# Performance work log

Measured on AMD Instinct MI355X. Metric: run time of the kernel, lower is better.

Reference implementation:

```python
import jax, jax.numpy as jnp
import numpy as np

NUM_HEADS = 32
NUM_KV_HEADS = 8  # num_heads // 4 (GQA)
HEAD_DIM = 64     # hidden_size // num_heads
ROPE_BASE = 10000.0


def _rotate_half(x):
    x1, x2 = jnp.split(x, 2, axis=-1)
    return jnp.concatenate((-x2, x1), axis=-1)


def _rope_cos_sin(seq_len, dtype):
    inv_freq = 1.0 / (ROPE_BASE ** (jnp.arange(0, HEAD_DIM, 2, dtype=jnp.float32) / HEAD_DIM))
    t = jnp.arange(seq_len, dtype=jnp.float32)
    freqs = jnp.outer(t, inv_freq)                 # [S, HEAD_DIM//2]
    emb = jnp.concatenate((freqs, freqs), axis=-1) # [S, HEAD_DIM]
    return jnp.cos(emb).astype(dtype), jnp.sin(emb).astype(dtype)


def setup_inputs() -> dict:
    key = jax.random.key(0)
    ks = jax.random.split(key, 5)
    B, S, H = 1, 2048, 2048
    KV = NUM_KV_HEADS * HEAD_DIM  # 512
    s = 0.02
    return {
        "hidden_states": jax.random.normal(ks[0], (B, S, H), jnp.float32),
        "Wq": jax.random.normal(ks[1], (H, H), jnp.float32) * s,
        "Wk": jax.random.normal(ks[2], (KV, H), jnp.float32) * s,
        "Wv": jax.random.normal(ks[3], (KV, H), jnp.float32) * s,
        "Wo": jax.random.normal(ks[4], (H, H), jnp.float32) * s,
    }


def reference(hidden_states, Wq, Wk, Wv, Wo):
    B, S, H = hidden_states.shape
    dtype = hidden_states.dtype
    # QKV projections (nn.Linear with weight [out,in], no bias)
    q = jnp.einsum("bsh,oh->bso", hidden_states, Wq)
    k = jnp.einsum("bsh,oh->bso", hidden_states, Wk)
    v = jnp.einsum("bsh,oh->bso", hidden_states, Wv)
    q = q.reshape(B, S, NUM_HEADS, HEAD_DIM).transpose(0, 2, 1, 3)      # [B,H,S,D]
    k = k.reshape(B, S, NUM_KV_HEADS, HEAD_DIM).transpose(0, 2, 1, 3)   # [B,KV,S,D]
    v = v.reshape(B, S, NUM_KV_HEADS, HEAD_DIM).transpose(0, 2, 1, 3)
    # RoPE
    cos, sin = _rope_cos_sin(S, dtype)  # [S,D] broadcast over batch/heads
    q = q * cos + _rotate_half(q) * sin
    k = k * cos + _rotate_half(k) * sin
    # GQA: repeat_interleave KV heads
    groups = NUM_HEADS // NUM_KV_HEADS
    k = jnp.repeat(k, groups, axis=1)
    v = jnp.repeat(v, groups, axis=1)
    # Attention: scores in fp32 softmax, causal mask (additive)
    scale = 1.0 / np.sqrt(HEAD_DIM)
    scores = jnp.einsum("bhqd,bhkd->bhqk", q, k) * scale
    causal = jnp.tril(jnp.ones((S, S), dtype=bool))
    scores = jnp.where(causal, scores, jnp.finfo(jnp.float32).min)
    probs = jax.nn.softmax(scores.astype(jnp.float32), axis=-1).astype(dtype)
    attn = jnp.einsum("bhqk,bhkd->bhqd", probs, v)
    attn = attn.transpose(0, 2, 1, 3).reshape(B, S, H)
    return jnp.einsum("bsh,oh->bso", attn, Wo)
```

## Files before the change

### kernel.cpp

```cpp
#include <hip/hip_runtime.h>
#include <hip/hip_bf16.h>
#include <math.h>

typedef __hip_bfloat16 bf16;
typedef __attribute__((ext_vector_type(8))) short short8;
typedef __attribute__((ext_vector_type(4))) short short4v;
typedef __attribute__((ext_vector_type(4))) float floatx4;

#define MFMA16(a, b, c) __builtin_amdgcn_mfma_f32_16x16x32_bf16((a), (b), (c), 0, 0, 0)

typedef const __attribute__((address_space(1))) void* as1_cvp;
typedef __attribute__((address_space(3))) void* as3_vp;

__device__ __forceinline__ void gload_lds16(const bf16* g, bf16* lds_uni) {
    __builtin_amdgcn_global_load_lds((as1_cvp)g, (as3_vp)lds_uni, 16, 0, 0);
}

__global__ __launch_bounds__(256) void cvt_all(
    const float* __restrict__ a0, const float* __restrict__ a1,
    const float* __restrict__ a2, const float* __restrict__ a3,
    const float* __restrict__ a4,
    bf16* __restrict__ d0, bf16* __restrict__ d1, bf16* __restrict__ d2,
    bf16* __restrict__ d3, bf16* __restrict__ d4)
{
    const int b = blockIdx.x;
    const float* src; bf16* dst; int off;
    if (b < 2048)      { src = a0; dst = d0; off = b; }
    else if (b < 4096) { src = a1; dst = d1; off = b - 2048; }
    else if (b < 4608) { src = a2; dst = d2; off = b - 4096; }
    else if (b < 5120) { src = a3; dst = d3; off = b - 4608; }
    else               { src = a4; dst = d4; off = b - 5120; }
    const int i = (off * 256 + threadIdx.x) * 8;
    const float4 x = *(const float4*)(src + i);
    const float4 y = *(const float4*)(src + i + 4);
    bf16 t[8];
    t[0] = __float2bfloat16(x.x); t[1] = __float2bfloat16(x.y);
    t[2] = __float2bfloat16(x.z); t[3] = __float2bfloat16(x.w);
    t[4] = __float2bfloat16(y.x); t[5] = __float2bfloat16(y.y);
    t[6] = __float2bfloat16(y.z); t[7] = __float2bfloat16(y.w);
    *(short8*)(dst + i) = *(const short8*)t;
}

#define GEMM_STAGE6(k0, sA, sB)                                                 \
    gload_lds16(gA + (k0),            (sA));                                    \
    gload_lds16(gA + A64 + (k0),      (sA) + 2048);                             \
    gload_lds16(gB + (k0),            (sB));                                    \
    gload_lds16(gA + (k0) + 32,       (sA) + 4096);                             \
    gload_lds16(gA + A64 + (k0) + 32, (sA) + 6144);                             \
    gload_lds16(gB + (k0) + 32,       (sB) + 2048);

#define GEMM_K_LOOP_DB(KB)                                                      \
    {                                                                           \
        bf16* sA0 = &As[0][0] + w * 512; bf16* sB0 = &Bs[0][0] + w * 512;       \
        bf16* sA1 = &As[1][0] + w * 512; bf16* sB1 = &Bs[1][0] + w * 512;       \
        GEMM_STAGE6(0, sA0, sB0)                                                \
        for (int k0 = 0; k0 < (KB); k0 += 64) {                                 \
            const int cur = (k0 >> 6) & 1;                                      \
            if (k0 + 64 < (KB)) {                                               \
                if (cur == 0) { GEMM_STAGE6(k0 + 64, sA1, sB1) }                \
                else          { GEMM_STAGE6(k0 + 64, sA0, sB0) }                \
                asm volatile("s_waitcnt vmcnt(6)" ::: "memory");                \
            } else {                                                            \
                asm volatile("s_waitcnt vmcnt(0)" ::: "memory");                \
            }                                                                   \
            __builtin_amdgcn_s_barrier();                                       \
            const bf16* Acur = &As[cur][0];                                     \
            const bf16* Bcur = &Bs[cur][0];                                     \
            _Pragma("unroll")                                                   \
            for (int hh = 0; hh < 2; ++hh) {                                    \
                short8 af[2], bfr[4];                                           \
                _Pragma("unroll")                                               \
                for (int i = 0; i < 2; ++i)                                     \
                    af[i] = *(const short8*)&Acur[hh * 4096 + (w * 32 + i * 16 + l15) * 32 + quad * 8]; \
                _Pragma("unroll")                                               \
                for (int j = 0; j < 4; ++j)                                     \
                    bfr[j] = *(const short8*)&Bcur[hh * 2048 + (j * 16 + l15) * 32 + quad * 8]; \
                _Pragma("unroll")                                               \
                for (int i = 0; i < 2; ++i)                                     \
                    _Pragma("unroll")                                           \
                    for (int j = 0; j < 4; ++j)                                 \
                        acc[i][j] = MFMA16(af[i], bfr[j], acc[i][j]);           \
            }                                                                   \
            __builtin_amdgcn_s_barrier();                                       \
        }                                                                       \
    }

__global__ __launch_bounds__(256) void gemm_qkv(
    const bf16* __restrict__ A, const bf16* __restrict__ Wq,
    const bf16* __restrict__ Wk, const bf16* __restrict__ Wv,
    bf16* __restrict__ qb, bf16* __restrict__ kb, bf16* __restrict__ vt)
{
    constexpr int LDK = 2048;
    __shared__ bf16 As[2][128 * 64];
    __shared__ bf16 Bs[2][64 * 64];

    const int tid  = threadIdx.x;
    const int lane = tid & 63;
    const int w    = tid >> 6;
    const int quad = lane >> 4, l15 = lane & 15;
    const int bx = blockIdx.x, by = blockIdx.y;

    const bf16* Bp; int bxl, mode;
    if (bx < 32)      { Bp = Wq; bxl = bx;      mode = 0; }
    else if (bx < 40) { Bp = Wk; bxl = bx - 32; mode = 1; }
    else              { Bp = Wv; bxl = bx - 40; mode = 2; }

    floatx4 acc[2][4];
#pragma unroll
    for (int i = 0; i < 2; ++i)
#pragma unroll
        for (int j = 0; j < 4; ++j) {
            floatx4 z = {0.f, 0.f, 0.f, 0.f};
            acc[i][j] = z;
        }

    const int srow = tid >> 2;
    const int sch  = (tid & 3) * 8;
    const bf16* gA = A  + (size_t)(by * 128 + srow) * LDK + sch;
    const bf16* gB = Bp + (size_t)(bxl * 64 + srow) * LDK + sch;
    const size_t A64 = (size_t)64 * LDK;

    GEMM_K_LOOP_DB(LDK)

    if (mode == 2) {
#pragma unroll
        for (int i = 0; i < 2; ++i)
#pragma unroll
            for (int j = 0; j < 4; ++j) {
                const int col = bxl * 64 + j * 16 + l15;
                const int rowb = by * 128 + w * 32 + i * 16 + quad * 4;
                bf16 t[4];
#pragma unroll
                for (int r = 0; r < 4; ++r) t[r] = __float2bfloat16(acc[i][j][r]);
                *(short4v*)&vt[(size_t)col * 2048 + rowb] = *(const short4v*)t;
            }
    } else {
        bf16* C = (mode == 0) ? qb : kb;
        const int Nn = (mode == 0) ? 2048 : 512;
        const float scale = (mode == 0) ? 0.125f : 1.0f;
        const float LOG2_1E4 = 13.28771237954945f;
        const float ifr0 = exp2f(-((float)l15) * (LOG2_1E4 / 32.f));
        const float ifr1 = exp2f(-((float)(16 + l15)) * (LOG2_1E4 / 32.f));
#pragma unroll
        for (int i = 0; i < 2; ++i) {
#pragma unroll
            for (int r = 0; r < 4; ++r) {
                const int row = by * 128 + w * 32 + i * 16 + quad * 4 + r;
                float s0, c0, s1, c1;
                sincosf((float)row * ifr0, &s0, &c0);
                sincosf((float)row * ifr1, &s1, &c1);
#pragma unroll
                for (int j = 0; j < 4; ++j) {
                    const float x  = acc[i][j][r];
                    const float xp = acc[i][j ^ 2][r];
                    const float cs = (j & 1) ? c1 : c0;
                    const float sn = (j & 1) ? s1 : s0;
                    const float oo = (x * cs + ((j < 2) ? -xp : xp) * sn) * scale;
                    const int col = bxl * 64 + j * 16 + l15;
                    C[(size_t)row * Nn + col] = __float2bfloat16(oo);
                }
            }
        }
    }
}

__global__ __launch_bounds__(256) void gemm_out(
    const bf16* __restrict__ A, const bf16* __restrict__ B, float* __restrict__ C)
{
    constexpr int LDK = 2048;
    __shared__ bf16 As[2][128 * 64];
    __shared__ bf16 Bs[2][64 * 64];

    const int tid  = threadIdx.x;
    const int lane = tid & 63;
    const int w    = tid >> 6;
    const int quad = lane >> 4, l15 = lane & 15;
    const int bx = blockIdx.x, by = blockIdx.y;

    floatx4 acc[2][4];
#pragma unroll
    for (int i = 0; i < 2; ++i)
#pragma unroll
        for (int j = 0; j < 4; ++j) {
            floatx4 z = {0.f, 0.f, 0.f, 0.f};
            acc[i][j] = z;
        }

    const int srow = tid >> 2;
    const int sch  = (tid & 3) * 8;
    const bf16* gA = A + (size_t)(by * 128 + srow) * LDK + sch;
    const bf16* gB = B + (size_t)(bx * 64 + srow) * LDK + sch;
    const size_t A64 = (size_t)64 * LDK;

    GEMM_K_LOOP_DB(LDK)

#pragma unroll
    for (int i = 0; i < 2; ++i)
#pragma unroll
        for (int j = 0; j < 4; ++j)
#pragma unroll
            for (int r = 0; r < 4; ++r) {
                const int row = by * 128 + w * 32 + i * 16 + quad * 4 + r;
                const int col = bx * 64 + j * 16 + l15;
                C[(size_t)row * 2048 + col] = acc[i][j][r];
            }
}

__global__ __launch_bounds__(256) void fattn4b(
    const bf16* __restrict__ q, const bf16* __restrict__ k,
    const bf16* __restrict__ vt, bf16* __restrict__ o)
{
    __shared__ bf16 Ks[2][64 * 72];
    __shared__ bf16 Vs[2][64 * 72];
    __shared__ bf16 Ps[4][16 * 68];

    const int tpair = blockIdx.x;
    const int h = blockIdx.y;
    const int kvh = h >> 2;
    const int tid = threadIdx.x, lane = tid & 63, w = tid >> 6;
    const int quad = lane >> 4, l15 = lane & 15;
    bf16* P = Ps[w];

    short ob[8];
#pragma unroll
    for (int e = 0; e < 8; ++e) ob[e] = (short)0x3F80;
    const short8 ones = *(const short8*)ob;

    const int srow = tid >> 3;
    const int ch8  = (tid & 7) * 8;
    const bf16* kg = k  + (size_t)kvh * 64 + ch8;
    const bf16* vg = vt + (size_t)(kvh * 64 + srow) * 2048 + ch8;

#pragma unroll 1
    for (int ph = 0; ph < 2; ++ph) {
        const int a = ph ? (31 - tpair) : tpair;
        const int qrow0 = a * 64 + w * 16;

        short8 qf[2];
#pragma unroll
        for (int ks = 0; ks < 2; ++ks)
            qf[ks] = *(const short8*)&q[(size_t)(qrow0 + l15) * 2048 + h * 64 + ks * 32 + quad * 8];

        floatx4 o_acc[4], l_acc;
#pragma unroll
        for (int n4 = 0; n4 < 4; ++n4) {
            floatx4 z = {0.f, 0.f, 0.f, 0.f};
            o_acc[n4] = z;
        }
        { floatx4 z = {0.f, 0.f, 0.f, 0.f}; l_acc = z; }

        {
            short8 k0 = *(const short8*)(kg + (size_t)srow * 512);
            short8 k1 = *(const short8*)(kg + (size_t)(srow + 32) * 512);
            short8 v0 = *(const short8*)(vg);
            short8 v1 = *(const short8*)(vg + (size_t)32 * 2048);
            *(short8*)&Ks[0][srow * 72 + ch8]        = k0;
            *(short8*)&Ks[0][(srow + 32) * 72 + ch8] = k1;
            *(short8*)&Vs[0][srow * 72 + ch8]        = v0;
            *(short8*)&Vs[0][(srow + 32) * 72 + ch8] = v1;
        }
        __syncthreads();

        for (int kt = 0; kt <= a; ++kt) {
            const int buf = kt & 1;

            short8 nk0, nk1, nv0, nv1;
            if (kt < a) {
                const size_t kr = (size_t)((kt + 1) * 64) * 512;
                nk0 = *(const short8*)(kg + kr + (size_t)srow * 512);
                nk1 = *(const short8*)(kg + kr + (size_t)(srow + 32) * 512);
                nv0 = *(const short8*)(vg + (kt + 1) * 64);
                nv1 = *(const short8*)(vg + (size_t)32 * 2048 + (kt + 1) * 64);
            }

            floatx4 s_acc[4];
#pragma unroll
            for (int n = 0; n < 4; ++n) {
                floatx4 z = {0.f, 0.f, 0.f, 0.f};
                s_acc[n] = z;
            }
#pragma unroll
            for (int n = 0; n < 4; ++n)
#pragma unroll
                for (int ks = 0; ks < 2; ++ks) {
                    const short8 kf = *(const short8*)&Ks[buf][(n * 16 + l15) * 72 + ks * 32 + quad * 8];
                    s_acc[n] = MFMA16(kf, qf[ks], s_acc[n]);
                }

            if (kt < a) {
#pragma unroll
                for (int n = 0; n < 4; ++n) {
                    bf16 t4[4];
#pragma unroll
                    for (int r = 0; r < 4; ++r)
                        t4[r] = __float2bfloat16(__expf(s_acc[n][r]));
                    *(short4v*)&P[l15 * 68 + n * 16 + quad * 4] = *(const short4v*)t4;
                }
            } else {
#pragma unroll
                for (int n = 0; n < 4; ++n) {
                    bf16 t4[4];
#pragma unroll
                    for (int r = 0; r < 4; ++r) {
                        const bool okc = (n * 16 + quad * 4 + r) <= (w * 16 + l15);
                        t4[r] = __float2bfloat16(okc ? __expf(s_acc[n][r]) : 0.f);
                    }
                    *(short4v*)&P[l15 * 68 + n * 16 + quad * 4] = *(const short4v*)t4;
                }
            }

#pragma unroll
            for (int ks2 = 0; ks2 < 2; ++ks2) {
                const short8 pf = *(const short8*)&P[l15 * 68 + ks2 * 32 + quad * 8];
                l_acc = MFMA16(pf, ones, l_acc);
#pragma unroll
                for (int n4 = 0; n4 < 4; ++n4) {
                    const short8 vf = *(const short8*)&Vs[buf][(n4 * 16 + l15) * 72 + ks2 * 32 + quad * 8];
                    o_acc[n4] = MFMA16(pf, vf, o_acc[n4]);
                }
            }

            if (kt < a) {
                *(short8*)&Ks[buf ^ 1][srow * 72 + ch8]        = nk0;
                *(short8*)&Ks[buf ^ 1][(srow + 32) * 72 + ch8] = nk1;
                *(short8*)&Vs[buf ^ 1][srow * 72 + ch8]        = nv0;
                *(short8*)&Vs[buf ^ 1][(srow + 32) * 72 + ch8] = nv1;
            }
            __syncthreads();
        }

#pragma unroll
        for (int n4 = 0; n4 < 4; ++n4)
#pragma unroll
            for (int r = 0; r < 4; ++r) {
                const float val = o_acc[n4][r] / l_acc[r];
                const int row = qrow0 + quad * 4 + r;
                const int col = h * 64 + n4 * 16 + l15;
                o[(size_t)row * 2048 + col] = __float2bfloat16(val);
            }
    }
}

extern "C" void kernel_launch(void* const* d_in, const int* in_sizes, int n_in,
                              void* d_out, int out_size, void* d_ws, size_t ws_size,
                              hipStream_t stream)
{
    const float* hs = (const float*)d_in[0];
    const float* Wq = (const float*)d_in[1];
    const float* Wk = (const float*)d_in[2];
    const float* Wv = (const float*)d_in[3];
    const float* Wo = (const float*)d_in[4];
    float* out = (float*)d_out;

    bf16* ws  = (bf16*)d_ws;
    bf16* hsb = ws;
    bf16* Wqb = ws + 4194304;
    bf16* Wkb = ws + 8388608;
    bf16* Wvb = ws + 9437184;
    bf16* Wob = ws + 10485760;
    bf16* qb  = ws + 14680064;
    bf16* kb  = ws + 18874368;
    bf16* vtb = ws + 19922944;
    bf16* ab  = ws + 20971520;

    dim3 blk(256);
    cvt_all<<<7168, blk, 0, stream>>>(hs, Wq, Wk, Wv, Wo, hsb, Wqb, Wkb, Wvb, Wob);
    gemm_qkv<<<dim3(48, 16), blk, 0, stream>>>(hsb, Wqb, Wkb, Wvb, qb, kb, vtb);
    fattn4b<<<dim3(16, 32), blk, 0, stream>>>(qb, kb, vtb, ab);
    gemm_out<<<dim3(32, 16), blk, 0, stream>>>(ab, Wob, out);
}
```

Before: 219.6 us.

## Rework attention to 512-thread blocks with 32x32 MFMA and 256-row query tiles

Measured after the change: 247.4 us. +12.7%, slower.

```diff
diff --git a/kernel.cpp b/kernel.cpp
--- a/kernel.cpp
+++ b/kernel.cpp
@@ -6,8 +6,10 @@
 typedef __attribute__((ext_vector_type(8))) short short8;
 typedef __attribute__((ext_vector_type(4))) short short4v;
 typedef __attribute__((ext_vector_type(4))) float floatx4;
+typedef __attribute__((ext_vector_type(16))) float floatx16;
 
 #define MFMA16(a, b, c) __builtin_amdgcn_mfma_f32_16x16x32_bf16((a), (b), (c), 0, 0, 0)
+#define MFMA32(a, b, c) __builtin_amdgcn_mfma_f32_32x32x16_bf16((a), (b), (c), 0, 0, 0)
 
 typedef const __attribute__((address_space(1))) void* as1_cvp;
 typedef __attribute__((address_space(3))) void* as3_vp;
@@ -206,138 +208,147 @@
             }
 }
 
-__global__ __launch_bounds__(256) void fattn4b(
+__global__ __launch_bounds__(512, 2) void fattn8(
     const bf16* __restrict__ q, const bf16* __restrict__ k,
     const bf16* __restrict__ vt, bf16* __restrict__ o)
 {
     __shared__ bf16 Ks[2][64 * 72];
     __shared__ bf16 Vs[2][64 * 72];
-    __shared__ bf16 Ps[4][16 * 68];
-
-    const int tpair = blockIdx.x;
-    const int h = blockIdx.y;
+    __shared__ bf16 Ps[8][32 * 68];
+
+    const int qp = blockIdx.x;
+    const int h  = blockIdx.y;
     const int kvh = h >> 2;
-    const int tid = threadIdx.x, lane = tid & 63, w = tid >> 6;
-    const int quad = lane >> 4, l15 = lane & 15;
+    const int tid = threadIdx.x;
+    const int lane = tid & 63, w = tid >> 6;
+    const int l31 = lane & 31, hl = lane >> 5;
     bf16* P = Ps[w];
-
-    short ob[8];
-#pragma unroll
-    for (int e = 0; e < 8; ++e) ob[e] = (short)0x3F80;
-    const short8 ones = *(const short8*)ob;
 
     const int srow = tid >> 3;
     const int ch8  = (tid & 7) * 8;
-    const bf16* kg = k  + (size_t)kvh * 64 + ch8;
-    const bf16* vg = vt + (size_t)(kvh * 64 + srow) * 2048 + ch8;
+    const bf16* kgp = k  + (size_t)srow * 512 + kvh * 64 + ch8;
+    const bf16* vg  = vt + (size_t)(kvh * 64 + srow) * 2048 + ch8;
 
 #pragma unroll 1
     for (int ph = 0; ph < 2; ++ph) {
-        const int a = ph ? (31 - tpair) : tpair;
-        const int qrow0 = a * 64 + w * 16;
-
-        short8 qf[2];
-#pragma unroll
-        for (int ks = 0; ks < 2; ++ks)
-            qf[ks] = *(const short8*)&q[(size_t)(qrow0 + l15) * 2048 + h * 64 + ks * 32 + quad * 8];
-
-        floatx4 o_acc[4], l_acc;
-#pragma unroll
-        for (int n4 = 0; n4 < 4; ++n4) {
-            floatx4 z = {0.f, 0.f, 0.f, 0.f};
-            o_acc[n4] = z;
-        }
-        { floatx4 z = {0.f, 0.f, 0.f, 0.f}; l_acc = z; }
+        const int a = ph ? (7 - qp) : qp;
+        const int nkt = 4 * a + 4;
+        const int qrow0 = a * 256 + w * 32;
+
+        short8 qf[4];
+#pragma unroll
+        for (int ks = 0; ks < 4; ++ks)
+            qf[ks] = *(const short8*)&q[(size_t)(qrow0 + l31) * 2048 + h * 64 + ks * 16 + hl * 8];
+
+        floatx16 o_acc[2];
+#pragma unroll
+        for (int dt = 0; dt < 2; ++dt)
+#pragma unroll
+            for (int i = 0; i < 16; ++i) o_acc[dt][i] = 0.f;
+        float lsum = 0.f;
 
         {
-            short8 k0 = *(const short8*)(kg + (size_t)srow * 512);
-            short8 k1 = *(const short8*)(kg + (size_t)(srow + 32) * 512);
+            short8 k0 = *(const short8*)(kgp);
             short8 v0 = *(const short8*)(vg);
-            short8 v1 = *(const short8*)(vg + (size_t)32 * 2048);
-            *(short8*)&Ks[0][srow * 72 + ch8]        = k0;
-            *(short8*)&Ks[0][(srow + 32) * 72 + ch8] = k1;
-            *(short8*)&Vs[0][srow * 72 + ch8]        = v0;
-            *(short8*)&Vs[0][(srow + 32) * 72 + ch8] = v1;
+            *(short8*)&Ks[0][srow * 72 + ch8] = k0;
+            *(short8*)&Vs[0][srow * 72 + ch8] = v0;
         }
         __syncthreads();
 
-        for (int kt = 0; kt <= a; ++kt) {
+        for (int kt = 0; kt < nkt; ++kt) {
             const int buf = kt & 1;
 
-            short8 nk0, nk1, nv0, nv1;
-            if (kt < a) {
-                const size_t kr = (size_t)((kt + 1) * 64) * 512;
-                nk0 = *(const short8*)(kg + kr + (size_t)srow * 512);
-                nk1 = *(const short8*)(kg + kr + (size_t)(srow + 32) * 512);
-                nv0 = *(const short8*)(vg + (kt + 1) * 64);
-                nv1 = *(const short8*)(vg + (size_t)32 * 2048 + (kt + 1) * 64);
-            }
-
-            floatx4 s_acc[4];
-#pragma unroll
-            for (int n = 0; n < 4; ++n) {
-                floatx4 z = {0.f, 0.f, 0.f, 0.f};
-                s_acc[n] = z;
-            }
-#pragma unroll
-            for (int n = 0; n < 4; ++n)
-#pragma unroll
-                for (int ks = 0; ks < 2; ++ks) {
-                    const short8 kf = *(const short8*)&Ks[buf][(n * 16 + l15) * 72 + ks * 32 + quad * 8];
-                    s_acc[n] = MFMA16(kf, qf[ks], s_acc[n]);
-                }
-
-            if (kt < a) {
-#pragma unroll
-                for (int n = 0; n < 4; ++n) {
-                    bf16 t4[4];
-#pragma unroll
-                    for (int r = 0; r < 4; ++r)
-                        t4[r] = __float2bfloat16(__expf(s_acc[n][r]));
-                    *(short4v*)&P[l15 * 68 + n * 16 + quad * 4] = *(const short4v*)t4;
-                }
-            } else {
-#pragma unroll
-                for (int n = 0; n < 4; ++n) {
-                    bf16 t4[4];
-#pragma unroll
-                    for (int r = 0; r < 4; ++r) {
-                        const bool okc = (n * 16 + quad * 4 + r) <= (w * 16 + l15);
-                        t4[r] = __float2bfloat16(okc ? __expf(s_acc[n][r]) : 0.f);
-                    }
-                    *(short4v*)&P[l15 * 68 + n * 16 + quad * 4] = *(const short4v*)t4;
-                }
-            }
-
-#pragma unroll
-            for (int ks2 = 0; ks2 < 2; ++ks2) {
-                const short8 pf = *(const short8*)&P[l15 * 68 + ks2 * 32 + quad * 8];
-                l_acc = MFMA16(pf, ones, l_acc);
-#pragma unroll
-                for (int n4 = 0; n4 < 4; ++n4) {
-                    const short8 vf = *(const short8*)&Vs[buf][(n4 * 16 + l15) * 72 + ks2 * 32 + quad * 8];
-                    o_acc[n4] = MFMA16(pf, vf, o_acc[n4]);
-                }
-            }
-
-            if (kt < a) {
-                *(short8*)&Ks[buf ^ 1][srow * 72 + ch8]        = nk0;
-                *(short8*)&Ks[buf ^ 1][(srow + 32) * 72 + ch8] = nk1;
-                *(short8*)&Vs[buf ^ 1][srow * 72 + ch8]        = nv0;
-                *(short8*)&Vs[buf ^ 1][(srow + 32) * 72 + ch8] = nv1;
+            short8 nk, nv;
+            if (kt + 1 < nkt) {
+                nk = *(const short8*)(kgp + (size_t)(kt + 1) * 64 * 512);
+                nv = *(const short8*)(vg + (kt + 1) * 64);
+            }
+
+            const bool skip = (kt * 64 > qrow0 + 31);
+            if (!skip) {
+                const bool full = (kt * 64 + 63 <= qrow0);
+
+                floatx16 sa[2];
+#pragma unroll
+                for (int st = 0; st < 2; ++st)
+#pragma unroll
+                    for (int i = 0; i < 16; ++i) sa[st][i] = 0.f;
+#pragma unroll
+                for (int ks = 0; ks < 4; ++ks) {
+                    const short8 kf0 = *(const short8*)&Ks[buf][(l31)      * 72 + ks * 16 + hl * 8];
+                    const short8 kf1 = *(const short8*)&Ks[buf][(32 + l31) * 72 + ks * 16 + hl * 8];
+                    sa[0] = MFMA32(kf0, qf[ks], sa[0]);
+                    sa[1] = MFMA32(kf1, qf[ks], sa[1]);
+                }
+
+                if (full) {
+#pragma unroll
+                    for (int st = 0; st < 2; ++st)
+#pragma unroll
+                        for (int g = 0; g < 4; ++g) {
+                            bf16 t4[4];
+#pragma unroll
+                            for (int e = 0; e < 4; ++e) {
+                                const float ex = __expf(sa[st][g * 4 + e]);
+                                t4[e] = __float2bfloat16(ex);
+                                lsum += __bfloat162float(t4[e]);
+                            }
+                            *(short4v*)&P[l31 * 68 + st * 32 + g * 8 + hl * 4] = *(const short4v*)t4;
+                        }
+                } else {
+                    const int qg = qrow0 + l31;
+#pragma unroll
+                    for (int st = 0; st < 2; ++st)
+#pragma unroll
+                        for (int g = 0; g < 4; ++g) {
+                            bf16 t4[4];
+#pragma unroll
+                            for (int e = 0; e < 4; ++e) {
+                                const int sg = kt * 64 + st * 32 + e + 8 * g + 4 * hl;
+                                const float ex = (sg <= qg) ? __expf(sa[st][g * 4 + e]) : 0.f;
+                                t4[e] = __float2bfloat16(ex);
+                                lsum += __bfloat162float(t4[e]);
+                            }
+                            *(short4v*)&P[l31 * 68 + st * 32 + g * 8 + hl * 4] = *(const short4v*)t4;
+                        }
+                }
+
+#pragma unroll
+                for (int ks = 0; ks < 4; ++ks) {
+                    const short8 pa  = *(const short8*)&P[l31 * 68 + ks * 16 + hl * 8];
+                    const short8 vf0 = *(const short8*)&Vs[buf][(l31)      * 72 + ks * 16 + hl * 8];
+                    const short8 vf1 = *(const short8*)&Vs[buf][(32 + l31) * 72 + ks * 16 + hl * 8];
+                    o_acc[0] = MFMA32(pa, vf0, o_acc[0]);
+                    o_acc[1] = MFMA32(pa, vf1, o_acc[1]);
+                }
+            }
+
+            if (kt + 1 < nkt) {
+                *(short8*)&Ks[buf ^ 1][srow * 72 + ch8] = nk;
+                *(short8*)&Vs[buf ^ 1][srow * 72 + ch8] = nv;
             }
             __syncthreads();
         }
 
-#pragma unroll
-        for (int n4 = 0; n4 < 4; ++n4)
-#pragma unroll
-            for (int r = 0; r < 4; ++r) {
-                const float val = o_acc[n4][r] / l_acc[r];
-                const int row = qrow0 + quad * 4 + r;
-                const int col = h * 64 + n4 * 16 + l15;
-                o[(size_t)row * 2048 + col] = __float2bfloat16(val);
-            }
+        const float lf = lsum + __shfl_xor(lsum, 32, 64);
+        float denom[16];
+#pragma unroll
+        for (int g = 0; g < 4; ++g)
+#pragma unroll
+            for (int e = 0; e < 4; ++e)
+                denom[g * 4 + e] = __shfl(lf, e + 8 * g + 4 * hl, 64);
+
+#pragma unroll
+        for (int dt = 0; dt < 2; ++dt)
+#pragma unroll
+            for (int g = 0; g < 4; ++g)
+#pragma unroll
+                for (int e = 0; e < 4; ++e) {
+                    const int r = g * 4 + e;
+                    const int row = qrow0 + e + 8 * g + 4 * hl;
+                    const int col = h * 64 + dt * 32 + l31;
+                    o[(size_t)row * 2048 + col] = __float2bfloat16(o_acc[dt][r] / denom[r]);
+                }
     }
 }
 
@@ -366,6 +377,6 @@
     dim3 blk(256);
     cvt_all<<<7168, blk, 0, stream>>>(hs, Wq, Wk, Wv, Wo, hsb, Wqb, Wkb, Wvb, Wob);
     gemm_qkv<<<dim3(48, 16), blk, 0, stream>>>(hsb, Wqb, Wkb, Wvb, qb, kb, vtb);
-    fattn4b<<<dim3(16, 32), blk, 0, stream>>>(qb, kb, vtb, ab);
+    fattn8<<<dim3(8, 32), dim3(512), 0, stream>>>(qb, kb, vtb, ab);
     gemm_out<<<dim3(32, 16), blk, 0, stream>>>(ab, Wob, out);
 }
```
